# Kernel tuning notes

Measured on AMD Instinct MI355X. Metric: run time of the kernel, lower is better.

Reference implementation:

```python
import jax, jax.numpy as jnp
import numpy as np

L, B, D = 2048, 8, 768
EPS_BN = 1e-5
EPS_LN = 1e-5
SCALE = 1.0 / float(np.sqrt(D))


def setup_inputs() -> dict:
    key = jax.random.key(0)
    ks = jax.random.split(key, 8)
    f32 = jnp.float32
    return {
        "x_a": jax.random.normal(ks[0], (L, B, D), dtype=f32),
        "x_v": jax.random.normal(ks[1], (L, B, D), dtype=f32),
        "x": jax.random.normal(ks[2], (L, B, D), dtype=f32),
        # conv1x1 (audio branch): weight [out_ch, in_ch], bias [out_ch]
        "W_a": jax.random.normal(ks[3], (D, D), dtype=f32) * 0.02,
        "b_a": jnp.zeros((D,), f32),
        "bn_a_g": jnp.ones((D,), f32),
        "bn_a_b": jnp.zeros((D,), f32),
        "prelu_a": jnp.full((1,), 0.25, f32),
        # conv1x1 (video branch)
        "W_v": jax.random.normal(ks[4], (D, D), dtype=f32) * 0.02,
        "b_v": jnp.zeros((D,), f32),
        "bn_v_g": jnp.ones((D,), f32),
        "bn_v_b": jnp.zeros((D,), f32),
        "prelu_v": jnp.full((1,), 0.25, f32),
        # final LayerNorm affine
        "ln_g": jnp.ones((D,), f32),
        "ln_b": jnp.zeros((D,), f32),
    }


def _branch(q, kv, W, b, bn_g, bn_b, alpha):
    # q: [B, L, D] queries; kv: [B, Lm, D] keys == values (cross-modal)
    attn = jax.nn.softmax(jnp.einsum('bld,bmd->blm', q, kv) * SCALE, axis=-1)
    ctx = jnp.einsum('blm,bmd->bld', attn, kv)            # [B, L, D]
    # Conv1d(kernel=1) over channel dim D == per-position linear
    y = jnp.einsum('bld,ed->ble', ctx, W) + b             # [B, L, D]
    # BatchNorm1d in training mode: batch stats over (B, L) per channel, biased var
    mean = jnp.mean(y, axis=(0, 1))
    var = jnp.var(y, axis=(0, 1))
    y = (y - mean) * jax.lax.rsqrt(var + EPS_BN) * bn_g + bn_b
    # PReLU (single shared alpha)
    return jnp.where(y > 0, y, alpha * y)


def reference(x_a, x_v, x, W_a, b_a, bn_a_g, bn_a_b, prelu_a,
              W_v, b_v, bn_v_g, bn_v_b, prelu_v, ln_g, ln_b):
    xa = jnp.swapaxes(x_a, 0, 1)   # [B, La, D]
    xv = jnp.swapaxes(x_v, 0, 1)   # [B, Lv, D]
    xq = jnp.swapaxes(x, 0, 1)     # [B, L, D]

    res_a = _branch(xq, xa, W_a, b_a, bn_a_g, bn_a_b, prelu_a)
    res_v = _branch(xq, xv, W_v, b_v, bn_v_g, bn_v_b, prelu_v)

    out = xq + res_a + res_v
    out = jnp.swapaxes(out, 0, 1)  # back to [L, B, D]

    mu = jnp.mean(out, axis=-1, keepdims=True)
    var = jnp.var(out, axis=-1, keepdims=True)
    return (out - mu) * jax.lax.rsqrt(var + EPS_LN) * ln_g + ln_b
```

## Files before the change

kernel.cpp:

```cpp
#include <hip/hip_runtime.h>
#include <stdint.h>

#define LL 2048
#define BB 8
#define DD 768
#define NROWS (LL*BB)
#define QKSCALE 0.03608439182435161f
#define EP 72

typedef __attribute__((ext_vector_type(8))) short short8;
typedef __attribute__((ext_vector_type(4))) float f32x4;
typedef unsigned short u16;
typedef unsigned int u32;

__device__ __forceinline__ float bf2f(u16 u) {
    union { u32 u; float f; } c; c.u = ((u32)u) << 16; return c.f;
}
__device__ __forceinline__ u16 f2bf(float f) {
    union { float f; u32 u; } c; c.f = f;
    return (u16)((c.u + 0x8000u) >> 16);
}

__global__ __launch_bounds__(256)
void cvt_kernel(const float* __restrict__ s0, u16* __restrict__ d0,
                const float* __restrict__ s1, u16* __restrict__ d1,
                const float* __restrict__ s2, u16* __restrict__ d2,
                const float* __restrict__ s3, u16* __restrict__ d3,
                const float* __restrict__ s4, u16* __restrict__ d4,
                int nbig4, int nsmall4)
{
    const float* src; u16* dst; int n4;
    switch (blockIdx.y) {
        case 0: src = s0; dst = d0; n4 = nbig4; break;
        case 1: src = s1; dst = d1; n4 = nbig4; break;
        case 2: src = s2; dst = d2; n4 = nbig4; break;
        case 3: src = s3; dst = d3; n4 = nsmall4; break;
        default: src = s4; dst = d4; n4 = nsmall4; break;
    }
    for (int i = blockIdx.x * 256 + threadIdx.x; i < n4; i += gridDim.x * 256) {
        float4 v = *(const float4*)&src[i * 4];
        ushort4 o;
        o.x = f2bf(v.x); o.y = f2bf(v.y); o.z = f2bf(v.z); o.w = f2bf(v.w);
        *(ushort4*)&dst[i * 4] = o;
    }
}

__device__ __forceinline__ void gll16(const u16* g, u16* l) {
    __builtin_amdgcn_global_load_lds((const __attribute__((address_space(1))) u32*)g,
                                     (__attribute__((address_space(3))) u32*)l, 16, 0, 0);
}

template<int EPI>
__global__ __launch_bounds__(512, 2)
void gemm_bt256(const u16* __restrict__ A, int lda, long astr,
                const u16* __restrict__ B, int ldb, long bstr,
                u16* __restrict__ C, long cstr, int ldc,
                int K, int sw,
                float* __restrict__ lsum,
                const float* __restrict__ bias,
                float* __restrict__ stats)
{
    __shared__ u16 lds[65536];

    const int tid = threadIdx.x;
    const int z = blockIdx.z;
    const int flat = blockIdx.y * gridDim.x + blockIdx.x;
    const int per = sw * gridDim.x;
    const int bm = (flat / per) * sw + (flat % sw);
    const int bn = (flat % per) / sw;
    const int m0 = bm * 256, n0 = bn * 256;

    const u16* Ab = A + (size_t)z * astr + (size_t)m0 * lda;
    const u16* Bb = B + (size_t)z * bstr + (size_t)n0 * ldb;
    u16* Cb = C + (size_t)z * cstr;

    const int lane = tid & 63, w = tid >> 6;
    const int wm = w >> 2, wn = w & 3;
    const int lr = lane & 15, lg = lane >> 4;

    const int ar0 = tid >> 2;
    const int ar1 = ar0 + 128;
    const int ag0 = (tid & 3) ^ ((ar0 >> 1) & 3);
    const int ag1 = (tid & 3) ^ ((ar1 >> 1) & 3);
    const u16* gA0 = Ab + (size_t)ar0 * lda + ag0 * 8;
    const u16* gA1 = Ab + (size_t)ar1 * lda + ag1 * 8;
    const u16* gB0 = Bb + (size_t)ar0 * ldb + ag0 * 8;
    const u16* gB1 = Bb + (size_t)ar1 * ldb + ag1 * 8;
    const int lA0 = tid * 8;
    const int lA1 = tid * 8 + 4096;
    const int lB0 = 8192 + tid * 8;
    const int lB1 = 12288 + tid * 8;

    const int swz = (lr >> 1) & 3;
    const int aoff = (wm * 128 + lr) * 32 + ((lg ^ swz) * 8);
    const int boff = 8192 + (wn * 64 + lr) * 32 + ((lg ^ swz) * 8);

    f32x4 acc[8][4];
    const f32x4 zz = {0.f, 0.f, 0.f, 0.f};
    #pragma unroll
    for (int i = 0; i < 8; ++i)
        #pragma unroll
        for (int j = 0; j < 4; ++j) acc[i][j] = zz;

    const int nt = K >> 5;

    short8 a1[4], a2[4], bE[4], bO[4];

    {
        u16* b0 = lds;
        u16* b1 = lds + 16384;
        gll16(gA0, b0 + lA0); gll16(gA1, b0 + lA1);
        gll16(gB0, b0 + lB0); gll16(gB1, b0 + lB1);
        gll16(gA0 + 32, b1 + lA0); gll16(gA1 + 32, b1 + lA1);
        gll16(gB0 + 32, b1 + lB0); gll16(gB1 + 32, b1 + lB1);
    }
    asm volatile("s_waitcnt vmcnt(4)" ::: "memory");
    asm volatile("s_barrier" ::: "memory");
    #pragma unroll
    for (int mi = 0; mi < 4; ++mi) a1[mi] = *(const short8*)&lds[aoff + mi * 512];
    #pragma unroll
    for (int ni = 0; ni < 4; ++ni) bE[ni] = *(const short8*)&lds[boff + ni * 512];

#define TILE_STEP(T, BC, BN)                                                            \
    {                                                                                   \
        const int cb_ = ((T) & 3) * 16384;                                              \
        const int sb_ = (((T) + 2) & 3) * 16384;                                        \
        const int kt2_ = ((T) + 2) * 32;                                                \
        _Pragma("unroll")                                                               \
        for (int mi = 0; mi < 4; ++mi)                                                  \
            a2[mi] = *(const short8*)&lds[cb_ + aoff + 2048 + mi * 512];                \
        if ((T) + 2 < nt) {                                                             \
            gll16(gA0 + kt2_, lds + sb_ + lA0);                                         \
            gll16(gA1 + kt2_, lds + sb_ + lA1);                                         \
        }                                                                               \
        __builtin_amdgcn_s_setprio(1);                                                  \
        _Pragma("unroll")                                                               \
        for (int mi = 0; mi < 4; ++mi)                                                  \
            _Pragma("unroll")                                                           \
            for (int ni = 0; ni < 4; ++ni)                                              \
                acc[mi][ni] = __builtin_amdgcn_mfma_f32_16x16x32_bf16(a1[mi], BC[ni], acc[mi][ni], 0, 0, 0); \
        __builtin_amdgcn_s_setprio(0);                                                  \
        if ((T) + 2 < nt) {                                                             \
            gll16(gB0 + kt2_, lds + sb_ + lB0);                                         \
            gll16(gB1 + kt2_, lds + sb_ + lB1);                                         \
        }                                                                               \
        if ((T) < nt - 2) { asm volatile("s_waitcnt vmcnt(4)" ::: "memory"); }          \
        else              { asm volatile("s_waitcnt vmcnt(0)" ::: "memory"); }          \
        asm volatile("s_barrier" ::: "memory");                                         \
        if ((T) + 1 < nt) {                                                             \
            const int nb_ = (((T) + 1) & 3) * 16384;                                    \
            _Pragma("unroll")                                                           \
            for (int mi = 0; mi < 4; ++mi)                                              \
                a1[mi] = *(const short8*)&lds[nb_ + aoff + mi * 512];                   \
            _Pragma("unroll")                                                           \
            for (int ni = 0; ni < 4; ++ni)                                              \
                BN[ni] = *(const short8*)&lds[nb_ + boff + ni * 512];                   \
        }                                                                               \
        __builtin_amdgcn_s_setprio(1);                                                  \
        _Pragma("unroll")                                                               \
        for (int mi = 0; mi < 4; ++mi)                                                  \
            _Pragma("unroll")                                                           \
            for (int ni = 0; ni < 4; ++ni)                                              \
                acc[mi + 4][ni] = __builtin_amdgcn_mfma_f32_16x16x32_bf16(a2[mi], BC[ni], acc[mi + 4][ni], 0, 0, 0); \
        __builtin_amdgcn_s_setprio(0);                                                  \
    }

    for (int t = 0; t < nt; t += 2) {
        TILE_STEP(t, bE, bO)
        TILE_STEP(t + 1, bO, bE)
    }
#undef TILE_STEP

    asm volatile("s_barrier" ::: "memory");
    u16* eb = lds + w * 4608;

    float invl[8][4]; float bcol[4];
    if constexpr (EPI == 2) {
        #pragma unroll
        for (int mi = 0; mi < 8; ++mi)
            #pragma unroll
            for (int r = 0; r < 4; ++r)
                invl[mi][r] = 1.0f / lsum[z * 2048 + m0 + wm * 128 + mi * 16 + lg * 4 + r];
        #pragma unroll
        for (int ni = 0; ni < 4; ++ni)
            bcol[ni] = bias[n0 + wn * 64 + ni * 16 + lr];
    }
    float csum[4] = {0, 0, 0, 0}, csq[4] = {0, 0, 0, 0};

    #pragma unroll
    for (int half = 0; half < 2; ++half) {
        #pragma unroll
        for (int mi = 0; mi < 4; ++mi) {
            const int MI = half * 4 + mi;
            float rsum[4] = {0, 0, 0, 0};
            #pragma unroll
            for (int ni = 0; ni < 4; ++ni) {
                #pragma unroll
                for (int r = 0; r < 4; ++r) {
                    float v = acc[MI][ni][r];
                    if constexpr (EPI == 1) { v = __expf(v * QKSCALE); rsum[r] += v; }
                    if constexpr (EPI == 2) { v = v * invl[MI][r] + bcol[ni]; csum[ni] += v; csq[ni] += v * v; }
                    eb[(mi * 16 + lg * 4 + r) * EP + ni * 16 + lr] = f2bf(v);
                }
            }
            if constexpr (EPI == 1) {
                #pragma unroll
                for (int r = 0; r < 4; ++r) {
                    float s = rsum[r];
                    s += __shfl_xor(s, 1); s += __shfl_xor(s, 2);
                    s += __shfl_xor(s, 4); s += __shfl_xor(s, 8);
                    if (lr == 0)
                        atomicAdd(&lsum[z * 2048 + m0 + wm * 128 + MI * 16 + lg * 4 + r], s);
                }
            }
        }
        #pragma unroll
        for (int c = 0; c < 8; ++c) {
            int row = c * 8 + (lane >> 3);
            short8 v = *(const short8*)&eb[row * EP + (lane & 7) * 8];
            *(short8*)&Cb[(size_t)(m0 + wm * 128 + half * 64 + row) * ldc + n0 + wn * 64 + (lane & 7) * 8] = v;
        }
    }
    if constexpr (EPI == 2) {
        #pragma unroll
        for (int ni = 0; ni < 4; ++ni) {
            float s = csum[ni], q = csq[ni];
            s += __shfl_xor(s, 16); s += __shfl_xor(s, 32);
            q += __shfl_xor(q, 16); q += __shfl_xor(q, 32);
            if (lg == 0) {
                atomicAdd(&stats[n0 + wn * 64 + ni * 16 + lr], s);
                atomicAdd(&stats[DD + n0 + wn * 64 + ni * 16 + lr], q);
            }
        }
    }
}

__global__ void bn_params(const float* __restrict__ stats_a, const float* __restrict__ stats_v,
                          const float* __restrict__ g_a, const float* __restrict__ be_a,
                          const float* __restrict__ g_v, const float* __restrict__ be_v,
                          float* __restrict__ bnp_a, float* __restrict__ bnp_v)
{
    const int e = threadIdx.x;
    const float* st = (blockIdx.x == 0) ? stats_a : stats_v;
    const float* g  = (blockIdx.x == 0) ? g_a  : g_v;
    const float* be = (blockIdx.x == 0) ? be_a : be_v;
    float* bnp = (blockIdx.x == 0) ? bnp_a : bnp_v;
    float mean = st[e] * (1.0f / NROWS);
    float var  = st[DD + e] * (1.0f / NROWS) - mean * mean;
    float scale = g[e] * rsqrtf(var + 1e-5f);
    bnp[e]      = scale;
    bnp[DD + e] = be[e] - mean * scale;
}

__global__ __launch_bounds__(256)
void final_kernel(const float* __restrict__ x,
                  const u16* __restrict__ y_a, const u16* __restrict__ y_v,
                  const float* __restrict__ bnp_a, const float* __restrict__ bnp_v,
                  const float* __restrict__ pra, const float* __restrict__ prv,
                  const float* __restrict__ lng, const float* __restrict__ lnb,
                  float* __restrict__ out)
{
    const int n = blockIdx.x;
    const int tid = threadIdx.x;
    __shared__ float vrow[DD];
    __shared__ float reds[4], reds2[4];
    const float aa = pra[0];
    const float av = prv[0];
    const size_t base = (size_t)n * DD;
    float s = 0.f, s2 = 0.f;
    for (int e = tid; e < DD; e += 256) {
        float ya = bf2f(y_a[base + e]) * bnp_a[e] + bnp_a[DD + e];
        ya = ya > 0.f ? ya : aa * ya;
        float yv = bf2f(y_v[base + e]) * bnp_v[e] + bnp_v[DD + e];
        yv = yv > 0.f ? yv : av * yv;
        float v = x[base + e] + ya + yv;
        vrow[e] = v;
        s += v; s2 += v * v;
    }
    for (int off = 32; off > 0; off >>= 1) { s += __shfl_xor(s, off); s2 += __shfl_xor(s2, off); }
    const int wv = tid >> 6;
    if ((tid & 63) == 0) { reds[wv] = s; reds2[wv] = s2; }
    __syncthreads();
    float ts  = reds[0] + reds[1] + reds[2] + reds[3];
    float ts2 = reds2[0] + reds2[1] + reds2[2] + reds2[3];
    float mean = ts * (1.0f / DD);
    float var  = ts2 * (1.0f / DD) - mean * mean;
    float rstd = rsqrtf(var + 1e-5f);
    for (int e = tid; e < DD; e += 256) {
        float o = (vrow[e] - mean) * rstd * lng[e] + lnb[e];
        out[base + e] = o;
    }
}

extern "C" void kernel_launch(void* const* d_in, const int* in_sizes, int n_in,
                              void* d_out, int out_size, void* d_ws, size_t ws_size,
                              hipStream_t stream)
{
    const float* x_a    = (const float*)d_in[0];
    const float* x_v    = (const float*)d_in[1];
    const float* x      = (const float*)d_in[2];
    const float* W_a    = (const float*)d_in[3];
    const float* b_a    = (const float*)d_in[4];
    const float* bn_a_g = (const float*)d_in[5];
    const float* bn_a_b = (const float*)d_in[6];
    const float* pr_a   = (const float*)d_in[7];
    const float* W_v    = (const float*)d_in[8];
    const float* b_v    = (const float*)d_in[9];
    const float* bn_v_g = (const float*)d_in[10];
    const float* bn_v_b = (const float*)d_in[11];
    const float* pr_v   = (const float*)d_in[12];
    const float* ln_g   = (const float*)d_in[13];
    const float* ln_b   = (const float*)d_in[14];

    float* stats_a = (float*)d_ws;
    float* stats_v = stats_a + 1536;
    float* bnp_a   = stats_v + 1536;
    float* bnp_v   = bnp_a + 1536;
    float* lsum    = bnp_v + 1536;
    u16* xq_bf = (u16*)(lsum + 16 * 2048);
    u16* xa_bf = xq_bf + (size_t)NROWS * DD;
    u16* xv_bf = xa_bf + (size_t)NROWS * DD;
    u16* Wa_bf = xv_bf + (size_t)NROWS * DD;
    u16* Wv_bf = Wa_bf + (size_t)DD * DD;
    u16* UT    = Wv_bf + (size_t)DD * DD;
    u16* y_a = xa_bf;
    u16* y_v = xv_bf;
    size_t fixed_bytes = (size_t)((char*)UT - (char*)d_ws);

    int nb = 1;
    for (int cand = 8; cand >= 1; cand >>= 1) {
        size_t need = fixed_bytes + (size_t)cand * (3145728ull + 8388608ull);
        if (need <= ws_size) { nb = cand; break; }
    }
    u16* P = UT + (size_t)nb * (768 * 2048);

    hipMemsetAsync(stats_a, 0, (4 * 1536 + 16 * 2048) * sizeof(float), stream);

    cvt_kernel<<<dim3(3072, 5), 256, 0, stream>>>(
        x, xq_bf, x_a, xa_bf, x_v, xv_bf, W_a, Wa_bf, W_v, Wv_bf,
        NROWS * DD / 4, DD * DD / 4);

    const u16*   KVs[2]   = { xa_bf, xv_bf };
    const u16*   Ws[2]    = { Wa_bf, Wv_bf };
    const float* BIs[2]   = { b_a, b_v };
    u16*         Ys[2]    = { y_a, y_v };
    float*       STs[2]   = { stats_a, stats_v };

    for (int br = 0; br < 2; ++br) {
        const u16* kv = KVs[br];
        for (int c0 = 0; c0 < 8; c0 += nb) {
            float* lsum_bc = (nb == 8) ? (lsum + br * 8 * 2048) : lsum;
            if (nb != 8)
                hipMemsetAsync(lsum, 0, (size_t)nb * 2048 * sizeof(float), stream);
            gemm_bt256<0><<<dim3(8, 3, nb), 512, 0, stream>>>(
                Ws[br], DD, 0, kv + c0 * DD, BB * DD, DD,
                UT, (long)768 * 2048, 2048, DD, 3, nullptr, nullptr, nullptr);
            gemm_bt256<1><<<dim3(8, 8, nb), 512, 0, stream>>>(
                xq_bf + c0 * DD, BB * DD, DD, kv + c0 * DD, BB * DD, DD,
                P, (long)2048 * 2048, 2048, DD, 4, lsum_bc, nullptr, nullptr);
            gemm_bt256<2><<<dim3(3, 8, nb), 512, 0, stream>>>(
                P, 2048, (long)2048 * 2048, UT, 2048, (long)768 * 2048,
                Ys[br] + (size_t)c0 * DD, DD, BB * DD, 2048, 4, lsum_bc, BIs[br], STs[br]);
        }
    }

    bn_params<<<2, 768, 0, stream>>>(stats_a, stats_v, bn_a_g, bn_a_b, bn_v_g, bn_v_b, bnp_a, bnp_v);
    final_kernel<<<NROWS, 256, 0, stream>>>(x, y_a, y_v, bnp_a, bnp_v, pr_a, pr_v, ln_g, ln_b,
                                            (float*)d_out);
}
```

Baseline: 571.0 us.

## Restructure GEMM main loop to 64-wide K tiles with quadrant-staged loads

Replaces the 4-stage 32-wide K pipeline with a double-buffered 64-wide K tile, using an 8-way XOR swizzle in LDS. Each tile is split into four MFMA quadrants, with partial global-to-LDS loads interleaved between barriers. A and B loads are staggered by one tile. The aim is to halve loop iterations and overlap loads with MFMA work more finely, at the cost of more barriers and lgkmcnt waits per tile.

```diff
diff --git a/kernel.cpp b/kernel.cpp
--- a/kernel.cpp
+++ b/kernel.cpp
@@ -78,22 +78,21 @@
     const int wm = w >> 2, wn = w & 3;
     const int lr = lane & 15, lg = lane >> 4;
 
-    const int ar0 = tid >> 2;
-    const int ar1 = ar0 + 128;
-    const int ag0 = (tid & 3) ^ ((ar0 >> 1) & 3);
-    const int ag1 = (tid & 3) ^ ((ar1 >> 1) & 3);
-    const u16* gA0 = Ab + (size_t)ar0 * lda + ag0 * 8;
-    const u16* gA1 = Ab + (size_t)ar1 * lda + ag1 * 8;
-    const u16* gB0 = Bb + (size_t)ar0 * ldb + ag0 * 8;
-    const u16* gB1 = Bb + (size_t)ar1 * ldb + ag1 * 8;
-    const int lA0 = tid * 8;
-    const int lA1 = tid * 8 + 4096;
-    const int lB0 = 8192 + tid * 8;
-    const int lB1 = 12288 + tid * 8;
-
-    const int swz = (lr >> 1) & 3;
-    const int aoff = (wm * 128 + lr) * 32 + ((lg ^ swz) * 8);
-    const int boff = 8192 + (wn * 64 + lr) * 32 + ((lg ^ swz) * 8);
+    const int tr = tid >> 3;
+    const int sg = (tid & 7) ^ ((tid >> 3) & 7);
+    const u16* pA = Ab + (size_t)tr * lda + sg * 8;
+    const u16* pB = Bb + (size_t)tr * ldb + sg * 8;
+    const size_t lda64 = (size_t)64 * lda;
+    const size_t ldb64 = (size_t)64 * ldb;
+
+    const int sl0 = (lg) ^ (lr & 7);
+    const int sl1 = (4 + lg) ^ (lr & 7);
+    const int aro = wm * 128 + lr;
+    const int bro = wn * 64 + lr;
+    const int aof0 = aro * 64 + sl0 * 8;
+    const int aof1 = aro * 64 + sl1 * 8;
+    const int bof0 = 16384 + bro * 64 + sl0 * 8;
+    const int bof1 = 16384 + bro * 64 + sl1 * 8;
 
     f32x4 acc[8][4];
     const f32x4 zz = {0.f, 0.f, 0.f, 0.f};
@@ -102,76 +101,128 @@
         #pragma unroll
         for (int j = 0; j < 4; ++j) acc[i][j] = zz;
 
-    const int nt = K >> 5;
-
-    short8 a1[4], a2[4], bE[4], bO[4];
-
-    {
-        u16* b0 = lds;
-        u16* b1 = lds + 16384;
-        gll16(gA0, b0 + lA0); gll16(gA1, b0 + lA1);
-        gll16(gB0, b0 + lB0); gll16(gB1, b0 + lB1);
-        gll16(gA0 + 32, b1 + lA0); gll16(gA1 + 32, b1 + lA1);
-        gll16(gB0 + 32, b1 + lB0); gll16(gB1 + 32, b1 + lB1);
-    }
+    const int nt = K >> 6;
+
+    short8 af[4][2], b01[2][2], b23[2][2];
+
+    gll16(pA,             lds + tid * 8);
+    gll16(pA + lda64,     lds + 4096 + tid * 8);
+    gll16(pA + 2 * lda64, lds + 8192 + tid * 8);
+    gll16(pA + 3 * lda64, lds + 12288 + tid * 8);
+    gll16(pB,             lds + 16384 + tid * 8);
+    gll16(pB + ldb64,     lds + 20480 + tid * 8);
+    gll16(pB + 2 * ldb64, lds + 24576 + tid * 8);
+    gll16(pB + 3 * ldb64, lds + 28672 + tid * 8);
+    gll16(pB + 64,             lds + 32768 + 16384 + tid * 8);
+    gll16(pB + 64 + ldb64,     lds + 32768 + 20480 + tid * 8);
+    gll16(pB + 64 + 2 * ldb64, lds + 32768 + 24576 + tid * 8);
+    gll16(pB + 64 + 3 * ldb64, lds + 32768 + 28672 + tid * 8);
     asm volatile("s_waitcnt vmcnt(4)" ::: "memory");
     asm volatile("s_barrier" ::: "memory");
-    #pragma unroll
-    for (int mi = 0; mi < 4; ++mi) a1[mi] = *(const short8*)&lds[aoff + mi * 512];
-    #pragma unroll
-    for (int ni = 0; ni < 4; ++ni) bE[ni] = *(const short8*)&lds[boff + ni * 512];
-
-#define TILE_STEP(T, BC, BN)                                                            \
+
+#define LGKM0()  do { asm volatile("s_waitcnt lgkmcnt(0)" ::: "memory"); \
+                      __builtin_amdgcn_sched_barrier(0); } while (0)
+#define BARR()   asm volatile("s_barrier" ::: "memory")
+
+#define TILE(T, DB, STA, STB, VM)                                                       \
     {                                                                                   \
-        const int cb_ = ((T) & 3) * 16384;                                              \
-        const int sb_ = (((T) + 2) & 3) * 16384;                                        \
-        const int kt2_ = ((T) + 2) * 32;                                                \
-        _Pragma("unroll")                                                               \
-        for (int mi = 0; mi < 4; ++mi)                                                  \
-            a2[mi] = *(const short8*)&lds[cb_ + aoff + 2048 + mi * 512];                \
-        if ((T) + 2 < nt) {                                                             \
-            gll16(gA0 + kt2_, lds + sb_ + lA0);                                         \
-            gll16(gA1 + kt2_, lds + sb_ + lA1);                                         \
+        const int T_ = (T);                                                             \
+        const u16* sA = pA + (size_t)(T_ + 1) * 64;                                     \
+        const u16* sB = pB + (size_t)(T_ + 2) * 64;                                     \
+        const int DBX = (DB) ^ 32768;                                                   \
+            \
+        _Pragma("unroll")                                                               \
+        for (int mi = 0; mi < 4; ++mi) {                                                \
+            af[mi][0] = *(const short8*)&lds[(DB) + aof0 + mi * 1024];                  \
+            af[mi][1] = *(const short8*)&lds[(DB) + aof1 + mi * 1024];                  \
         }                                                                               \
+        _Pragma("unroll")                                                               \
+        for (int ni = 0; ni < 2; ++ni) {                                                \
+            b01[ni][0] = *(const short8*)&lds[(DB) + bof0 + ni * 1024];                 \
+            b01[ni][1] = *(const short8*)&lds[(DB) + bof1 + ni * 1024];                 \
+        }                                                                               \
+        if (STA) { gll16(sA, lds + DBX + tid * 8);                                      \
+                   gll16(sA + lda64, lds + DBX + 4096 + tid * 8); }                     \
+        BARR();                                                                         \
+        LGKM0();                                                                        \
         __builtin_amdgcn_s_setprio(1);                                                  \
         _Pragma("unroll")                                                               \
         for (int mi = 0; mi < 4; ++mi)                                                  \
             _Pragma("unroll")                                                           \
-            for (int ni = 0; ni < 4; ++ni)                                              \
-                acc[mi][ni] = __builtin_amdgcn_mfma_f32_16x16x32_bf16(a1[mi], BC[ni], acc[mi][ni], 0, 0, 0); \
+            for (int ni = 0; ni < 2; ++ni) {                                            \
+                acc[mi][ni] = __builtin_amdgcn_mfma_f32_16x16x32_bf16(af[mi][0], b01[ni][0], acc[mi][ni], 0, 0, 0); \
+                acc[mi][ni] = __builtin_amdgcn_mfma_f32_16x16x32_bf16(af[mi][1], b01[ni][1], acc[mi][ni], 0, 0, 0); \
+            }                                                                           \
         __builtin_amdgcn_s_setprio(0);                                                  \
-        if ((T) + 2 < nt) {                                                             \
-            gll16(gB0 + kt2_, lds + sb_ + lB0);                                         \
-            gll16(gB1 + kt2_, lds + sb_ + lB1);                                         \
+        BARR();                                                                         \
+                                   \
+        _Pragma("unroll")                                                               \
+        for (int ni = 0; ni < 2; ++ni) {                                                \
+            b23[ni][0] = *(const short8*)&lds[(DB) + bof0 + 2048 + ni * 1024];          \
+            b23[ni][1] = *(const short8*)&lds[(DB) + bof1 + 2048 + ni * 1024];          \
         }                                                                               \
-        if ((T) < nt - 2) { asm volatile("s_waitcnt vmcnt(4)" ::: "memory"); }          \
-        else              { asm volatile("s_waitcnt vmcnt(0)" ::: "memory"); }          \
-        asm volatile("s_barrier" ::: "memory");                                         \
-        if ((T) + 1 < nt) {                                                             \
-            const int nb_ = (((T) + 1) & 3) * 16384;                                    \
-            _Pragma("unroll")                                                           \
-            for (int mi = 0; mi < 4; ++mi)                                              \
-                a1[mi] = *(const short8*)&lds[nb_ + aoff + mi * 512];                   \
-            _Pragma("unroll")                                                           \
-            for (int ni = 0; ni < 4; ++ni)                                              \
-                BN[ni] = *(const short8*)&lds[nb_ + boff + ni * 512];                   \
-        }                                                                               \
+        if (STA) { gll16(sA + 2 * lda64, lds + DBX + 8192 + tid * 8);                   \
+                   gll16(sA + 3 * lda64, lds + DBX + 12288 + tid * 8); }                \
+        BARR();                                                                         \
+        LGKM0();                                                                        \
         __builtin_amdgcn_s_setprio(1);                                                  \
         _Pragma("unroll")                                                               \
         for (int mi = 0; mi < 4; ++mi)                                                  \
             _Pragma("unroll")                                                           \
-            for (int ni = 0; ni < 4; ++ni)                                              \
-                acc[mi + 4][ni] = __builtin_amdgcn_mfma_f32_16x16x32_bf16(a2[mi], BC[ni], acc[mi + 4][ni], 0, 0, 0); \
+            for (int ni = 0; ni < 2; ++ni) {                                            \
+                acc[mi][ni + 2] = __builtin_amdgcn_mfma_f32_16x16x32_bf16(af[mi][0], b23[ni][0], acc[mi][ni + 2], 0, 0, 0); \
+                acc[mi][ni + 2] = __builtin_amdgcn_mfma_f32_16x16x32_bf16(af[mi][1], b23[ni][1], acc[mi][ni + 2], 0, 0, 0); \
+            }                                                                           \
         __builtin_amdgcn_s_setprio(0);                                                  \
-    }
-
-    for (int t = 0; t < nt; t += 2) {
-        TILE_STEP(t, bE, bO)
-        TILE_STEP(t + 1, bO, bE)
-    }
-#undef TILE_STEP
-
-    asm volatile("s_barrier" ::: "memory");
+        BARR();                                                                         \
+                       \
+        _Pragma("unroll")                                                               \
+        for (int mi = 0; mi < 4; ++mi) {                                                \
+            af[mi][0] = *(const short8*)&lds[(DB) + aof0 + 4096 + mi * 1024];           \
+            af[mi][1] = *(const short8*)&lds[(DB) + aof1 + 4096 + mi * 1024];           \
+        }                                                                               \
+        if (STB) { gll16(sB, lds + (DB) + 16384 + tid * 8);                             \
+                   gll16(sB + ldb64, lds + (DB) + 20480 + tid * 8); }                   \
+        BARR();                                                                         \
+        LGKM0();                                                                        \
+        __builtin_amdgcn_s_setprio(1);                                                  \
+        _Pragma("unroll")                                                               \
+        for (int mi = 0; mi < 4; ++mi)                                                  \
+            _Pragma("unroll")                                                           \
+            for (int ni = 0; ni < 2; ++ni) {                                            \
+                acc[mi + 4][ni] = __builtin_amdgcn_mfma_f32_16x16x32_bf16(af[mi][0], b01[ni][0], acc[mi + 4][ni], 0, 0, 0); \
+                acc[mi + 4][ni] = __builtin_amdgcn_mfma_f32_16x16x32_bf16(af[mi][1], b01[ni][1], acc[mi + 4][ni], 0, 0, 0); \
+            }                                                                           \
+        __builtin_amdgcn_s_setprio(0);                                                  \
+        BARR();                                                                         \
+         \
+        if (STB) { gll16(sB + 2 * ldb64, lds + (DB) + 24576 + tid * 8);                 \
+                   gll16(sB + 3 * ldb64, lds + (DB) + 28672 + tid * 8); }               \
+        if ((VM) == 4)      { asm volatile("s_waitcnt vmcnt(4)" ::: "memory"); }        \
+        else if ((VM) == 0) { asm volatile("s_waitcnt vmcnt(0)" ::: "memory"); }        \
+        BARR();                                                                         \
+        __builtin_amdgcn_s_setprio(1);                                                  \
+        _Pragma("unroll")                                                               \
+        for (int mi = 0; mi < 4; ++mi)                                                  \
+            _Pragma("unroll")                                                           \
+            for (int ni = 0; ni < 2; ++ni) {                                            \
+                acc[mi + 4][ni + 2] = __builtin_amdgcn_mfma_f32_16x16x32_bf16(af[mi][0], b23[ni][0], acc[mi + 4][ni + 2], 0, 0, 0); \
+                acc[mi + 4][ni + 2] = __builtin_amdgcn_mfma_f32_16x16x32_bf16(af[mi][1], b23[ni][1], acc[mi + 4][ni + 2], 0, 0, 0); \
+            }                                                                           \
+        __builtin_amdgcn_s_setprio(0);                                                  \
+        BARR();                                                                         \
+    }
+
+    for (int t = 0; t + 2 < nt; t += 2) {
+        TILE(t, 0, 1, 1, 4)
+        TILE(t + 1, 32768, 1, 1, 4)
+    }
+    TILE(nt - 2, 0, 1, 0, 0)
+    TILE(nt - 1, 32768, 0, 0, -1)
+#undef TILE
+#undef LGKM0
+#undef BARR
+
     u16* eb = lds + w * 4608;
 
     float invl[8][4]; float bcol[4];
```

Result: faster. 531.8 us (-6.9%).
